# Kernel tuning notes

Hardware: AMD Instinct MI355X
Metric: run time of the kernel (lower is better)

The kernel has to match this reference:

```python
import jax, jax.numpy as jnp
import numpy as np

B, N, L, E, R = 16384, 1024, 3, 8, 64


def _xavier(key, shape):
    # torch xavier_normal_ on (E, a, b): fan_in=b, fan_out=a (last two dims)
    fan_in, fan_out = shape[-1], shape[-2]
    std = float(np.sqrt(2.0 / (fan_in + fan_out)))
    return jax.random.normal(key, shape, dtype=jnp.float32) * std


def setup_inputs() -> dict:
    key = jax.random.key(0)
    ks = jax.random.split(key, 6)
    x = jax.random.normal(ks[0], (B, N), dtype=jnp.float32)
    U = _xavier(ks[1], (L, E, N, R))   # U_kernels per layer
    V = _xavier(ks[2], (L, E, R, N))   # V_kernels per layer
    C = _xavier(ks[3], (L, E, R, R))   # C_kernels per layer
    bias = jnp.zeros((L, N), dtype=jnp.float32)
    # gate Linear(N, 1, bias=False) per expert; torch default init kaiming_uniform
    bound = float(1.0 / np.sqrt(N))
    gate_w = jax.random.uniform(ks[4], (E, N), dtype=jnp.float32,
                                minval=-bound, maxval=bound)
    return {"x": x, "U": U, "V": V, "C": C, "bias": bias, "gate_w": gate_w}


def reference(x, U, V, C, bias, gate_w):
    x0 = x                                     # [B, N]
    x_l = x0
    for l in range(L):
        # gating logits per expert: [B, E], softmax over experts
        gates = jax.nn.softmax(jnp.einsum('bn,en->be', x_l, gate_w), axis=1)
        # low-rank expert chain, vectorized over experts
        v = jnp.einsum('ern,bn->ber', V[l], x_l)            # [B, E, R]
        c = jnp.einsum('ers,bes->ber', C[l], jax.nn.relu(v))  # [B, E, R]
        u = jnp.einsum('enr,ber->ben', U[l], jax.nn.relu(c))  # [B, E, N]
        experts = x0[:, None, :] * (u + bias[l][None, None, :])  # [B, E, N]
        moe = jnp.einsum('ben,be->bn', experts, gates)        # [B, N]
        x_l = moe + x_l
    return x_l
```

## Files before the change

### kernel.cpp

```cpp
#include <hip/hip_runtime.h>
#include <hip/hip_bf16.h>
#include <stdint.h>
#include <stddef.h>

typedef __bf16 bf16;
typedef __bf16 bf16x4 __attribute__((ext_vector_type(4)));
typedef __bf16 bf16x8 __attribute__((ext_vector_type(8)));
typedef float f32x4 __attribute__((ext_vector_type(4)));

#define BROWS 16384
#define NDIM 1024
#define NLAYERS 3
#define NEXP 8
#define RDIM 64

__device__ __forceinline__ void gld_lds16(const bf16* g, bf16* l) {
    __builtin_amdgcn_global_load_lds(
        (const __attribute__((address_space(1))) void*)g,
        (__attribute__((address_space(3))) void*)l, 16, 0, 0);
}

__global__ __launch_bounds__(256) void cvt_bf16_kernel(
    const float* __restrict__ src, bf16* __restrict__ dst, int n4)
{
    int i = blockIdx.x * 256 + threadIdx.x;
    if (i < n4) {
        float4 v = ((const float4*)src)[i];
        bf16x4 b;
        b[0] = (bf16)v.x; b[1] = (bf16)v.y; b[2] = (bf16)v.z; b[3] = (bf16)v.w;
        ((bf16x4*)dst)[i] = b;
    }
}

__global__ __launch_bounds__(256) void wu_transpose_kernel(
    const float* __restrict__ U, bf16* __restrict__ wu)
{
    int d = blockIdx.x * 256 + threadIdx.x;
    int r = d & 63;
    int e = (d >> 6) & 7;
    int n = (d >> 9) & 1023;
    int l = d >> 19;
    size_t s = (((size_t)(l * 8 + e)) * 1024 + n) * 64 + r;
    wu[d] = (bf16)U[s];
}

__global__ __launch_bounds__(256) void gates_xb_kernel(
    const float* __restrict__ xl, const float* __restrict__ gw,
    float* __restrict__ gates, bf16* __restrict__ xb)
{
    __shared__ float gs[NEXP * NDIM];
    const int tid = threadIdx.x;
#pragma unroll
    for (int i = 0; i < 8; ++i) {
        int f = (i * 256 + tid) * 4;
        *(float4*)&gs[f] = *(const float4*)&gw[f];
    }
    __syncthreads();
    const int wv = tid >> 6, ln = tid & 63;
    const int row = blockIdx.x * 4 + wv;
    const float* xr = xl + (size_t)row * NDIM;
    bf16* xbr = xb + (size_t)row * NDIM;

    float acc[8] = {0, 0, 0, 0, 0, 0, 0, 0};
#pragma unroll
    for (int i = 0; i < 4; ++i) {
        int n0 = (i * 64 + ln) * 4;
        float4 xv = *(const float4*)&xr[n0];
        bf16x4 bv;
        bv[0] = (bf16)xv.x; bv[1] = (bf16)xv.y; bv[2] = (bf16)xv.z; bv[3] = (bf16)xv.w;
        *(bf16x4*)&xbr[n0] = bv;
#pragma unroll
        for (int e = 0; e < 8; ++e) {
            const float* g4 = &gs[e * NDIM + n0];
            acc[e] += xv.x * g4[0] + xv.y * g4[1] + xv.z * g4[2] + xv.w * g4[3];
        }
    }
#pragma unroll
    for (int e = 0; e < 8; ++e) {
        float v = acc[e];
#pragma unroll
        for (int m = 32; m >= 1; m >>= 1) v += __shfl_xor(v, m);
        acc[e] = v;
    }
    float mx = acc[0];
#pragma unroll
    for (int e = 1; e < 8; ++e) mx = fmaxf(mx, acc[e]);
    float s = 0.f;
#pragma unroll
    for (int e = 0; e < 8; ++e) { acc[e] = __expf(acc[e] - mx); s += acc[e]; }
    float inv = 1.0f / s;
    if (ln == 0) {
#pragma unroll
        for (int e = 0; e < 8; ++e) gates[(size_t)row * 8 + e] = acc[e] * inv;
    }
}

template<int KDIM>
__global__ __launch_bounds__(256) void gemm_vc_kernel(
    const bf16* __restrict__ A, const bf16* __restrict__ Bt,
    const float* __restrict__ Cwl, const float* __restrict__ gates,
    bf16* __restrict__ cp)
{
    __shared__ __align__(16) bf16 smem[24576];
    bf16* As = smem;
    bf16* Bs = smem + 8192;
    bf16* Cs = smem + 16384;

    const int tid = threadIdx.x;
    const int wv = tid >> 6, ln = tid & 63;
    const long bm = (long)blockIdx.y * 128;
    const long bn = (long)blockIdx.x * 128;
    const int wm = (wv >> 1) << 6, wn = (wv & 1) << 6;
    const int e_loc = wv & 1;
    f32x4 acc[4][4] = {};

    {
        const float* Cg = Cwl + (size_t)(blockIdx.x * 2) * 4096;
#pragma unroll
        for (int i = 0; i < 8; ++i) {
            int f = tid * 32 + i * 4;
            float4 cv = *(const float4*)&Cg[f];
            int ee = f >> 12;
            int r  = (f >> 6) & 63;
            int s  = f & 63;
            bf16x4 b;
            b[0] = (bf16)cv.x; b[1] = (bf16)cv.y; b[2] = (bf16)cv.z; b[3] = (bf16)cv.w;
            char* base = (char*)Cs + ee * 8192;
            *(bf16x4*)(base + ((r * 128 + s * 2) ^ ((r & 7) << 4))) = b;
        }
    }

    const int srow = tid >> 3;
    const int scol = (tid & 7) * 8;
    const bf16* Abase = A + (bm + srow) * (long)KDIM + scol;
    const bf16* Bbase = Bt + (bn + srow) * (long)KDIM + scol;
    bf16* Asl = &As[(tid & ~63) * 8];
    bf16* Bsl = &Bs[(tid & ~63) * 8];

    for (int kt = 0; kt < KDIM / 64; ++kt) {
        const int k0 = kt * 64;
        __syncthreads();
#pragma unroll
        for (int t = 0; t < 4; ++t) {
            gld_lds16(Abase + (long)t * 32 * KDIM + k0, Asl + t * 2048);
            gld_lds16(Bbase + (long)t * 32 * KDIM + k0, Bsl + t * 2048);
        }
        __syncthreads();
#pragma unroll
        for (int kc = 0; kc < 2; ++kc) {
            bf16x8 af[4], bfr[4];
#pragma unroll
            for (int i = 0; i < 4; ++i) {
                af[i]  = *(const bf16x8*)&As[(wm + i * 16 + (ln & 15)) * 64 + kc * 32 + (ln >> 4) * 8];
                bfr[i] = *(const bf16x8*)&Bs[(wn + i * 16 + (ln & 15)) * 64 + kc * 32 + (ln >> 4) * 8];
            }
#pragma unroll
            for (int mi = 0; mi < 4; ++mi)
#pragma unroll
                for (int ni = 0; ni < 4; ++ni)
                    acc[mi][ni] = __builtin_amdgcn_mfma_f32_16x16x32_bf16(
                        af[mi], bfr[ni], acc[mi][ni], 0, 0, 0);
        }
    }

    __syncthreads();
    char* vsb = (char*)smem + wv * 8192;
    const int cr = (ln >> 4) * 4, cc = ln & 15;
#pragma unroll
    for (int mi = 0; mi < 4; ++mi)
#pragma unroll
        for (int ni = 0; ni < 4; ++ni)
#pragma unroll
            for (int j = 0; j < 4; ++j) {
                int row = mi * 16 + cr + j;
                int col = ni * 16 + cc;
                *(bf16*)(vsb + ((row * 128 + col * 2) ^ ((row & 7) << 4))) =
                    (bf16)fmaxf(acc[mi][ni][j], 0.f);
            }
    __syncthreads();

    f32x4 acc2[4][4] = {};
    char* csb = (char*)Cs + e_loc * 8192;
#pragma unroll
    for (int kc = 0; kc < 2; ++kc) {
        bf16x8 af[4], bfr[4];
        const int sb = (kc * 32 + (ln >> 4) * 8) * 2;
#pragma unroll
        for (int i = 0; i < 4; ++i) {
            int ra = i * 16 + (ln & 15);
            af[i]  = *(const bf16x8*)(vsb + ((ra * 128 + sb) ^ ((ra & 7) << 4)));
            bfr[i] = *(const bf16x8*)(csb + ((ra * 128 + sb) ^ ((ra & 7) << 4)));
        }
#pragma unroll
        for (int mi = 0; mi < 4; ++mi)
#pragma unroll
            for (int ni = 0; ni < 4; ++ni)
                acc2[mi][ni] = __builtin_amdgcn_mfma_f32_16x16x32_bf16(
                    af[mi], bfr[ni], acc2[mi][ni], 0, 0, 0);
    }

    const int e_g = (int)(bn >> 6) + e_loc;
#pragma unroll
    for (int mi = 0; mi < 4; ++mi)
#pragma unroll
        for (int j = 0; j < 4; ++j) {
            long row = bm + wm + mi * 16 + cr + j;
            float g = gates[row * 8 + e_g];
#pragma unroll
            for (int ni = 0; ni < 4; ++ni) {
                long col = bn + wn + ni * 16 + cc;
                cp[row * 512 + col] = (bf16)(fmaxf(acc2[mi][ni][j], 0.f) * g);
            }
        }
}

template<int KDIM>
__global__ __launch_bounds__(256) void gemm_kernel(
    const bf16* __restrict__ A, const bf16* __restrict__ Bt,
    const float* __restrict__ xl, const float* __restrict__ x0,
    const float* __restrict__ bias, float* __restrict__ out, int Ntot)
{
    __shared__ __align__(16) bf16 As[128 * 64];
    __shared__ __align__(16) bf16 Bs[128 * 64];
    const int tid = threadIdx.x;
    const int wv = tid >> 6, ln = tid & 63;
    const long bm = (long)blockIdx.y * 128;
    const long bn = (long)blockIdx.x * 128;
    const int wm = (wv >> 1) << 6, wn = (wv & 1) << 6;
    f32x4 acc[4][4] = {};

    const int srow = tid >> 3;
    const int scol = (tid & 7) * 8;
    const bf16* Abase = A + (bm + srow) * (long)KDIM + scol;
    const bf16* Bbase = Bt + (bn + srow) * (long)KDIM + scol;
    bf16* Asl = &As[(tid & ~63) * 8];
    bf16* Bsl = &Bs[(tid & ~63) * 8];

    for (int kt = 0; kt < KDIM / 64; ++kt) {
        const int k0 = kt * 64;
        __syncthreads();
#pragma unroll
        for (int t = 0; t < 4; ++t) {
            gld_lds16(Abase + (long)t * 32 * KDIM + k0, Asl + t * 2048);
            gld_lds16(Bbase + (long)t * 32 * KDIM + k0, Bsl + t * 2048);
        }
        __syncthreads();
#pragma unroll
        for (int kc = 0; kc < 2; ++kc) {
            bf16x8 af[4], bfr[4];
#pragma unroll
            for (int i = 0; i < 4; ++i) {
                af[i]  = *(const bf16x8*)&As[(wm + i * 16 + (ln & 15)) * 64 + kc * 32 + (ln >> 4) * 8];
                bfr[i] = *(const bf16x8*)&Bs[(wn + i * 16 + (ln & 15)) * 64 + kc * 32 + (ln >> 4) * 8];
            }
#pragma unroll
            for (int mi = 0; mi < 4; ++mi)
#pragma unroll
                for (int ni = 0; ni < 4; ++ni)
                    acc[mi][ni] = __builtin_amdgcn_mfma_f32_16x16x32_bf16(
                        af[mi], bfr[ni], acc[mi][ni], 0, 0, 0);
        }
    }

    const int cr = (ln >> 4) * 4, cc = ln & 15;
#pragma unroll
    for (int mi = 0; mi < 4; ++mi)
#pragma unroll
        for (int ni = 0; ni < 4; ++ni) {
            long col = bn + wn + ni * 16 + cc;
            float bcol = bias[col];
#pragma unroll
            for (int j = 0; j < 4; ++j) {
                long row = bm + wm + mi * 16 + cr + j;
                long idx = row * (long)Ntot + col;
                out[idx] = xl[idx] + x0[idx] * (acc[mi][ni][j] + bcol);
            }
        }
}

extern "C" void kernel_launch(void* const* d_in, const int* in_sizes, int n_in,
                              void* d_out, int out_size, void* d_ws, size_t ws_size,
                              hipStream_t stream)
{
    const float* x0   = (const float*)d_in[0];
    const float* U    = (const float*)d_in[1];
    const float* V    = (const float*)d_in[2];
    const float* Cw   = (const float*)d_in[3];
    const float* bias = (const float*)d_in[4];
    const float* gw   = (const float*)d_in[5];
    float* out = (float*)d_out;

    char* ws = (char*)d_ws;
    bf16*  wv    = (bf16*)ws;
    bf16*  wu    = (bf16*)(ws + 3145728);
    bf16*  xb    = (bf16*)(ws + 6291456);
    bf16*  cp    = (bf16*)(ws + 6291456 + 33554432);
    float* gates = (float*)(ws + 6291456 + 33554432 + 16777216);

    cvt_bf16_kernel<<<1536, 256, 0, stream>>>(V, wv, 393216);
    wu_transpose_kernel<<<6144, 256, 0, stream>>>(U, wu);

    for (int l = 0; l < NLAYERS; ++l) {
        const float* xl = (l == 0) ? x0 : out;
        gates_xb_kernel<<<4096, 256, 0, stream>>>(xl, gw, gates, xb);
        gemm_vc_kernel<1024><<<dim3(4, 128), 256, 0, stream>>>(
            xb, wv + (size_t)l * 524288, Cw + (size_t)l * 32768, gates, cp);
        gemm_kernel<512><<<dim3(8, 128), 256, 0, stream>>>(
            cp, wu + (size_t)l * 524288, xl, x0, bias + (size_t)l * 1024, out, 1024);
    }
}
```

Before: 409.0 us.

## Fuse gating softmax into V GEMM and emit bf16 activations from output epilogue

The separate per-layer gating/conversion kernel is removed. Gate logits are now computed inside the V-projection GEMM as an extra MFMA against a zero-padded bf16 copy of the gate weights, and the softmax is done in LDS. The output GEMM epilogue writes the bf16 copy of the next layer's input, reads x0 as bf16 instead of fp32, and uses a 128x64 tile for more blocks. This cuts a full read/write pass over the activations per layer. In exchange, gate logits and the x0 multiplier are computed in bf16 precision.

```diff
diff --git a/kernel.cpp b/kernel.cpp
--- a/kernel.cpp
+++ b/kernel.cpp
@@ -11,8 +11,6 @@
 #define BROWS 16384
 #define NDIM 1024
 #define NLAYERS 3
-#define NEXP 8
-#define RDIM 64
 
 __device__ __forceinline__ void gld_lds16(const bf16* g, bf16* l) {
     __builtin_amdgcn_global_load_lds(
@@ -44,67 +42,33 @@
     wu[d] = (bf16)U[s];
 }
 
-__global__ __launch_bounds__(256) void gates_xb_kernel(
-    const float* __restrict__ xl, const float* __restrict__ gw,
-    float* __restrict__ gates, bf16* __restrict__ xb)
-{
-    __shared__ float gs[NEXP * NDIM];
-    const int tid = threadIdx.x;
-#pragma unroll
-    for (int i = 0; i < 8; ++i) {
-        int f = (i * 256 + tid) * 4;
-        *(float4*)&gs[f] = *(const float4*)&gw[f];
-    }
-    __syncthreads();
-    const int wv = tid >> 6, ln = tid & 63;
-    const int row = blockIdx.x * 4 + wv;
-    const float* xr = xl + (size_t)row * NDIM;
-    bf16* xbr = xb + (size_t)row * NDIM;
-
-    float acc[8] = {0, 0, 0, 0, 0, 0, 0, 0};
-#pragma unroll
-    for (int i = 0; i < 4; ++i) {
-        int n0 = (i * 64 + ln) * 4;
-        float4 xv = *(const float4*)&xr[n0];
-        bf16x4 bv;
-        bv[0] = (bf16)xv.x; bv[1] = (bf16)xv.y; bv[2] = (bf16)xv.z; bv[3] = (bf16)xv.w;
-        *(bf16x4*)&xbr[n0] = bv;
-#pragma unroll
-        for (int e = 0; e < 8; ++e) {
-            const float* g4 = &gs[e * NDIM + n0];
-            acc[e] += xv.x * g4[0] + xv.y * g4[1] + xv.z * g4[2] + xv.w * g4[3];
-        }
-    }
-#pragma unroll
-    for (int e = 0; e < 8; ++e) {
-        float v = acc[e];
-#pragma unroll
-        for (int m = 32; m >= 1; m >>= 1) v += __shfl_xor(v, m);
-        acc[e] = v;
-    }
-    float mx = acc[0];
-#pragma unroll
-    for (int e = 1; e < 8; ++e) mx = fmaxf(mx, acc[e]);
-    float s = 0.f;
-#pragma unroll
-    for (int e = 0; e < 8; ++e) { acc[e] = __expf(acc[e] - mx); s += acc[e]; }
-    float inv = 1.0f / s;
-    if (ln == 0) {
-#pragma unroll
-        for (int e = 0; e < 8; ++e) gates[(size_t)row * 8 + e] = acc[e] * inv;
-    }
+__global__ __launch_bounds__(256) void gwp_kernel(
+    const float* __restrict__ gw, bf16* __restrict__ gwp)
+{
+    int d = (blockIdx.x * 256 + threadIdx.x) * 4;
+    int k  = d & 63;
+    int e  = (d >> 6) & 15;
+    int kt = d >> 10;
+    bf16x4 b = {};
+    if (e < 8) {
+        float4 v = *(const float4*)&gw[e * 1024 + kt * 64 + k];
+        b[0] = (bf16)v.x; b[1] = (bf16)v.y; b[2] = (bf16)v.z; b[3] = (bf16)v.w;
+    }
+    *(bf16x4*)&gwp[d] = b;
 }
 
 template<int KDIM>
 __global__ __launch_bounds__(256) void gemm_vc_kernel(
     const bf16* __restrict__ A, const bf16* __restrict__ Bt,
-    const float* __restrict__ Cwl, const float* __restrict__ gates,
+    const float* __restrict__ Cwl, const bf16* __restrict__ gwp,
     bf16* __restrict__ cp)
 {
-    __shared__ __align__(16) bf16 smem[24576];
+    __shared__ __align__(16) bf16 smem[27648];
     bf16* As = smem;
     bf16* Bs = smem + 8192;
     bf16* Cs = smem + 16384;
+    bf16* Gs = smem + 24576;
+    float* g_lds = (float*)(smem + 25600);
 
     const int tid = threadIdx.x;
     const int wv = tid >> 6, ln = tid & 63;
@@ -113,6 +77,7 @@
     const int wm = (wv >> 1) << 6, wn = (wv & 1) << 6;
     const int e_loc = wv & 1;
     f32x4 acc[4][4] = {};
+    f32x4 accg[4] = {};
 
     {
         const float* Cg = Cwl + (size_t)(blockIdx.x * 2) * 4096;
@@ -145,6 +110,10 @@
             gld_lds16(Abase + (long)t * 32 * KDIM + k0, Asl + t * 2048);
             gld_lds16(Bbase + (long)t * 32 * KDIM + k0, Bsl + t * 2048);
         }
+        if (wv == 3) {
+            gld_lds16(gwp + kt * 1024 + ln * 8, Gs);
+            gld_lds16(gwp + kt * 1024 + 512 + ln * 8, Gs + 512);
+        }
         __syncthreads();
 #pragma unroll
         for (int kc = 0; kc < 2; ++kc) {
@@ -160,12 +129,47 @@
                 for (int ni = 0; ni < 4; ++ni)
                     acc[mi][ni] = __builtin_amdgcn_mfma_f32_16x16x32_bf16(
                         af[mi], bfr[ni], acc[mi][ni], 0, 0, 0);
+            if ((wv & 1) == 0) {
+                bf16x8 gfr = *(const bf16x8*)&Gs[(ln & 15) * 64 + kc * 32 + (ln >> 4) * 8];
+#pragma unroll
+                for (int mi = 0; mi < 4; ++mi)
+                    accg[mi] = __builtin_amdgcn_mfma_f32_16x16x32_bf16(
+                        af[mi], gfr, accg[mi], 0, 0, 0);
+            }
         }
     }
 
     __syncthreads();
+
+    const int cr = (ln >> 4) * 4, cc = ln & 15;
+
+    if ((wv & 1) == 0) {
+#pragma unroll
+        for (int mi = 0; mi < 4; ++mi)
+#pragma unroll
+            for (int j = 0; j < 4; ++j) {
+                float l = accg[mi][j];
+                float m = l;
+#pragma unroll
+                for (int msk = 1; msk <= 4; msk <<= 1)
+                    m = fmaxf(m, __shfl_xor(l, msk));
+                float m2 = l;
+                m2 = fmaxf(m2, __shfl_xor(m2, 1));
+                m2 = fmaxf(m2, __shfl_xor(m2, 2));
+                m2 = fmaxf(m2, __shfl_xor(m2, 4));
+                float ex = __expf(l - m2);
+                float s = ex;
+                s += __shfl_xor(s, 1);
+                s += __shfl_xor(s, 2);
+                s += __shfl_xor(s, 4);
+                if (cc < 8) {
+                    int row = wm + mi * 16 + cr + j;
+                    g_lds[row * 8 + cc] = ex / s;
+                }
+            }
+    }
+
     char* vsb = (char*)smem + wv * 8192;
-    const int cr = (ln >> 4) * 4, cc = ln & 15;
 #pragma unroll
     for (int mi = 0; mi < 4; ++mi)
 #pragma unroll
@@ -199,13 +203,14 @@
                     af[mi], bfr[ni], acc2[mi][ni], 0, 0, 0);
     }
 
-    const int e_g = (int)(bn >> 6) + e_loc;
+    const int e_g = (int)(blockIdx.x * 2) + e_loc;
 #pragma unroll
     for (int mi = 0; mi < 4; ++mi)
 #pragma unroll
         for (int j = 0; j < 4; ++j) {
-            long row = bm + wm + mi * 16 + cr + j;
-            float g = gates[row * 8 + e_g];
+            int wrow = wm + mi * 16 + cr + j;
+            long row = bm + wrow;
+            float g = g_lds[wrow * 8 + e_g];
 #pragma unroll
             for (int ni = 0; ni < 4; ++ni) {
                 long col = bn + wn + ni * 16 + cc;
@@ -214,49 +219,52 @@
         }
 }
 
-template<int KDIM>
-__global__ __launch_bounds__(256) void gemm_kernel(
+template<bool XL_IS_X0, bool WRITE_XB>
+__global__ __launch_bounds__(256) void gemm2_kernel(
     const bf16* __restrict__ A, const bf16* __restrict__ Bt,
-    const float* __restrict__ xl, const float* __restrict__ x0,
-    const float* __restrict__ bias, float* __restrict__ out, int Ntot)
+    const float* __restrict__ xl, const bf16* __restrict__ xb0,
+    const float* __restrict__ bias, float* __restrict__ out,
+    bf16* __restrict__ xbn)
 {
     __shared__ __align__(16) bf16 As[128 * 64];
-    __shared__ __align__(16) bf16 Bs[128 * 64];
+    __shared__ __align__(16) bf16 Bs[64 * 64];
     const int tid = threadIdx.x;
     const int wv = tid >> 6, ln = tid & 63;
     const long bm = (long)blockIdx.y * 128;
-    const long bn = (long)blockIdx.x * 128;
-    const int wm = (wv >> 1) << 6, wn = (wv & 1) << 6;
-    f32x4 acc[4][4] = {};
+    const long bn = (long)blockIdx.x * 64;
+    const int wm = (wv >> 1) << 6, wn = (wv & 1) << 5;
+    f32x4 acc[4][2] = {};
 
     const int srow = tid >> 3;
     const int scol = (tid & 7) * 8;
-    const bf16* Abase = A + (bm + srow) * (long)KDIM + scol;
-    const bf16* Bbase = Bt + (bn + srow) * (long)KDIM + scol;
+    const bf16* Abase = A + (bm + srow) * 512L + scol;
+    const bf16* Bbase = Bt + (bn + srow) * 512L + scol;
     bf16* Asl = &As[(tid & ~63) * 8];
     bf16* Bsl = &Bs[(tid & ~63) * 8];
 
-    for (int kt = 0; kt < KDIM / 64; ++kt) {
+    for (int kt = 0; kt < 8; ++kt) {
         const int k0 = kt * 64;
         __syncthreads();
 #pragma unroll
-        for (int t = 0; t < 4; ++t) {
-            gld_lds16(Abase + (long)t * 32 * KDIM + k0, Asl + t * 2048);
-            gld_lds16(Bbase + (long)t * 32 * KDIM + k0, Bsl + t * 2048);
-        }
+        for (int t = 0; t < 4; ++t)
+            gld_lds16(Abase + (long)t * 32 * 512 + k0, Asl + t * 2048);
+#pragma unroll
+        for (int t = 0; t < 2; ++t)
+            gld_lds16(Bbase + (long)t * 32 * 512 + k0, Bsl + t * 2048);
         __syncthreads();
 #pragma unroll
         for (int kc = 0; kc < 2; ++kc) {
-            bf16x8 af[4], bfr[4];
-#pragma unroll
-            for (int i = 0; i < 4; ++i) {
+            bf16x8 af[4], bfr[2];
+#pragma unroll
+            for (int i = 0; i < 4; ++i)
                 af[i]  = *(const bf16x8*)&As[(wm + i * 16 + (ln & 15)) * 64 + kc * 32 + (ln >> 4) * 8];
+#pragma unroll
+            for (int i = 0; i < 2; ++i)
                 bfr[i] = *(const bf16x8*)&Bs[(wn + i * 16 + (ln & 15)) * 64 + kc * 32 + (ln >> 4) * 8];
-            }
 #pragma unroll
             for (int mi = 0; mi < 4; ++mi)
 #pragma unroll
-                for (int ni = 0; ni < 4; ++ni)
+                for (int ni = 0; ni < 2; ++ni)
                     acc[mi][ni] = __builtin_amdgcn_mfma_f32_16x16x32_bf16(
                         af[mi], bfr[ni], acc[mi][ni], 0, 0, 0);
         }
@@ -266,14 +274,18 @@
 #pragma unroll
     for (int mi = 0; mi < 4; ++mi)
 #pragma unroll
-        for (int ni = 0; ni < 4; ++ni) {
+        for (int ni = 0; ni < 2; ++ni) {
             long col = bn + wn + ni * 16 + cc;
             float bcol = bias[col];
 #pragma unroll
             for (int j = 0; j < 4; ++j) {
                 long row = bm + wm + mi * 16 + cr + j;
-                long idx = row * (long)Ntot + col;
-                out[idx] = xl[idx] + x0[idx] * (acc[mi][ni][j] + bcol);
+                long idx = row * 1024L + col;
+                float xlv = xl[idx];
+                float mul = XL_IS_X0 ? xlv : (float)xb0[idx];
+                float o = xlv + mul * (acc[mi][ni][j] + bcol);
+                out[idx] = o;
+                if (WRITE_XB) xbn[idx] = (bf16)o;
             }
         }
 }
@@ -291,21 +303,33 @@
     float* out = (float*)d_out;
 
     char* ws = (char*)d_ws;
-    bf16*  wv    = (bf16*)ws;
-    bf16*  wu    = (bf16*)(ws + 3145728);
-    bf16*  xb    = (bf16*)(ws + 6291456);
-    bf16*  cp    = (bf16*)(ws + 6291456 + 33554432);
-    float* gates = (float*)(ws + 6291456 + 33554432 + 16777216);
-
-    cvt_bf16_kernel<<<1536, 256, 0, stream>>>(V, wv, 393216);
+    bf16*  wvw  = (bf16*)ws;
+    bf16*  wu   = (bf16*)(ws + 3145728);
+    bf16*  gwp  = (bf16*)(ws + 6291456);
+    bf16*  xb0  = (bf16*)(ws + 6324224);
+    bf16*  xbn  = (bf16*)(ws + 6324224 + 33554432);
+    bf16*  cp   = (bf16*)(ws + 6324224 + 2 * 33554432);
+
+    cvt_bf16_kernel<<<1536, 256, 0, stream>>>(V, wvw, 393216);
+    cvt_bf16_kernel<<<16384, 256, 0, stream>>>(x0, xb0, 4194304);
     wu_transpose_kernel<<<6144, 256, 0, stream>>>(U, wu);
+    gwp_kernel<<<16, 256, 0, stream>>>(gw, gwp);
 
     for (int l = 0; l < NLAYERS; ++l) {
+        const bf16* xbl = (l == 0) ? xb0 : xbn;
         const float* xl = (l == 0) ? x0 : out;
-        gates_xb_kernel<<<4096, 256, 0, stream>>>(xl, gw, gates, xb);
         gemm_vc_kernel<1024><<<dim3(4, 128), 256, 0, stream>>>(
-            xb, wv + (size_t)l * 524288, Cw + (size_t)l * 32768, gates, cp);
-        gemm_kernel<512><<<dim3(8, 128), 256, 0, stream>>>(
-            cp, wu + (size_t)l * 524288, xl, x0, bias + (size_t)l * 1024, out, 1024);
-    }
-}
+            xbl, wvw + (size_t)l * 524288, Cw + (size_t)l * 32768, gwp, cp);
+        const bf16* wul = wu + (size_t)l * 524288;
+        const float* bl = bias + (size_t)l * 1024;
+        if (l == 0)
+            gemm2_kernel<true, true><<<dim3(16, 128), 256, 0, stream>>>(
+                cp, wul, xl, nullptr, bl, out, xbn);
+        else if (l == 1)
+            gemm2_kernel<false, true><<<dim3(16, 128), 256, 0, stream>>>(
+                cp, wul, xl, xb0, bl, out, xbn);
+        else
+            gemm2_kernel<false, false><<<dim3(16, 128), 256, 0, stream>>>(
+                cp, wul, xl, xb0, bl, out, nullptr);
+    }
+}
```

After: 422.3 us. 1.03x slower.
